# Performance work log

Measured on AMD Instinct MI355X. Metric: run time of the kernel, lower is better.

The kernel has to match this reference:

```python
import jax, jax.numpy as jnp
import numpy as np

NUM_HEADS = 8
D_MODEL = 512
D_K = D_MODEL // NUM_HEADS


def setup_inputs() -> dict:
    key = jax.random.key(0)
    ks = jax.random.split(key, 16)
    B, L, Dq = 4, 2048, 512
    s = 1.0 / np.sqrt(D_MODEL)
    inp = {
        "query": jax.random.normal(ks[0], (B, L, Dq), jnp.float32),
        "key": jax.random.normal(ks[1], (B, L, Dq), jnp.float32),
        "value": jax.random.normal(ks[2], (B, L, Dq), jnp.float32),
        "mask": jax.random.randint(ks[3], (B, L), 0, 2, jnp.int32),
        "Wq": jax.random.normal(ks[4], (Dq, D_MODEL), jnp.float32) * s,
        "bq": jax.random.normal(ks[5], (D_MODEL,), jnp.float32) * s,
        "Wk": jax.random.normal(ks[6], (Dq, D_MODEL), jnp.float32) * s,
        "bk": jax.random.normal(ks[7], (D_MODEL,), jnp.float32) * s,
        "Wv": jax.random.normal(ks[8], (Dq, D_MODEL), jnp.float32) * s,
        "bv": jax.random.normal(ks[9], (D_MODEL,), jnp.float32) * s,
        "Wo": jax.random.normal(ks[10], (D_MODEL, D_MODEL), jnp.float32) * s,
        "bo": jax.random.normal(ks[11], (D_MODEL,), jnp.float32) * s,
    }
    return inp


def _mha(query, key, value, mask, Wq, bq, Wk, bk, Wv, bv, Wo, bo):
    B, Q, _ = query.shape
    KV = key.shape[1]
    # projections, split into heads: (B, H, L, d_k)
    q = (query @ Wq + bq).reshape(B, Q, NUM_HEADS, D_K).transpose(0, 2, 1, 3)
    k = (key @ Wk + bk).reshape(B, KV, NUM_HEADS, D_K).transpose(0, 2, 1, 3)
    v = (value @ Wv + bv).reshape(B, KV, NUM_HEADS, D_K).transpose(0, 2, 1, 3)
    # full (B, H, Q, KV) score matrix, as in the original module
    scores = jnp.einsum("bhqd,bhkd->bhqk", q, k) / jnp.sqrt(jnp.asarray(D_K, q.dtype))
    m = (mask == 0)[:, None, None, :]  # (B,1,1,KV) broadcasting like unsqueeze(1)
    min_val = jnp.finfo(scores.dtype).min
    scores = jnp.where(m, min_val, scores)
    attn = jax.nn.softmax(scores, axis=-1)
    attn = jnp.where(m, 0.0, attn)
    xs = jnp.einsum("bhqk,bhkd->bhqd", attn, v)
    xs = xs.transpose(0, 2, 1, 3).reshape(B, Q, NUM_HEADS * D_K)
    return xs @ Wo + bo


def reference(query, key, value, mask, Wq, bq, Wk, bk, Wv, bv, Wo, bo):
    return _mha(query, key, value, mask, Wq, bq, Wk, bk, Wv, bv, Wo, bo)
```

## Files before the change

kernel.cpp:

```cpp
#include <hip/hip_runtime.h>
#include <math.h>

#define Bq 4
#define Lq 2048
#define NH 8
#define LDP6 36

typedef __attribute__((ext_vector_type(8))) __bf16 bf16x8;
typedef __attribute__((ext_vector_type(4))) float f32x4;
#define MFMA16(a,b,c) __builtin_amdgcn_mfma_f32_16x16x32_bf16(a,b,c,0,0,0)

__device__ __forceinline__ void async16(const void* g, void* l) {
    __builtin_amdgcn_global_load_lds(
        (const __attribute__((address_space(1))) unsigned int*)g,
        (__attribute__((address_space(3))) unsigned int*)l, 16, 0, 0);
}

__device__ __forceinline__ void splitbf(float x, ushort& h, ushort& l) {
    unsigned u = __float_as_uint(x);
    h = (ushort)(u >> 16);
    float hf = __uint_as_float(u & 0xffff0000u);
    l = (ushort)(__float_as_uint(x - hf) >> 16);
}
__device__ __forceinline__ ushort rnebf(float x) {
    unsigned u = __float_as_uint(x);
    return (ushort)((u + 0x7fffu + ((u >> 16) & 1u)) >> 16);
}

__global__ __launch_bounds__(256) void maskscan_kernel(
    const int* __restrict__ mask, int* __restrict__ idx, int* __restrict__ nvalid)
{
    __shared__ int ss[256];
    const int b = blockIdx.x, tid = threadIdx.x;
    int m[8], s = 0;
    #pragma unroll
    for (int j = 0; j < 8; ++j) { m[j] = (mask[b * 2048 + tid * 8 + j] != 0); s += m[j]; }
    int v = s;
    ss[tid] = v;
    __syncthreads();
    for (int off = 1; off < 256; off <<= 1) {
        int t_ = (tid >= off) ? ss[tid - off] : 0;
        __syncthreads();
        v += t_;
        ss[tid] = v;
        __syncthreads();
    }
    int pos = v - s;
    #pragma unroll
    for (int j = 0; j < 8; ++j) if (m[j]) idx[b * 2048 + pos++] = tid * 8 + j;
    int tot = ss[255];
    if (tid == 0) nvalid[b] = tot;
    for (int k = tot + tid; k < 2048; k += 256) idx[b * 2048 + k] = 0;
}

__global__ __launch_bounds__(256) void xsplit3_kernel(
    const float* __restrict__ X0, const float* __restrict__ X1, const float* __restrict__ X2,
    const int* __restrict__ idx,
    ushort* __restrict__ Xh, ushort* __restrict__ Xl)
{
    const int z = blockIdx.z;
    const float* X = (z == 0) ? X0 : (z == 1) ? X1 : X2;
    const size_t ebase = (size_t)blockIdx.x * 2048 + (size_t)threadIdx.x * 8;
    const int row = (int)(ebase >> 9), col = (int)(ebase & 511);
    const int b = row >> 11, r = row & 2047;
    const int srow = (z == 0) ? row : (b * 2048 + idx[b * 2048 + r]);
    const float* src = X + (size_t)srow * 512 + col;
    float4 a = *(const float4*)(src);
    float4 bb = *(const float4*)(src + 4);
    float vv[8] = {a.x, a.y, a.z, a.w, bb.x, bb.y, bb.z, bb.w};
    ushort hs[8], ls[8];
    #pragma unroll
    for (int j = 0; j < 8; ++j) splitbf(vv[j], hs[j], ls[j]);
    uint4 wh, wl;
    wh.x = hs[0] | ((unsigned)hs[1] << 16); wh.y = hs[2] | ((unsigned)hs[3] << 16);
    wh.z = hs[4] | ((unsigned)hs[5] << 16); wh.w = hs[6] | ((unsigned)hs[7] << 16);
    wl.x = ls[0] | ((unsigned)ls[1] << 16); wl.y = ls[2] | ((unsigned)ls[3] << 16);
    wl.z = ls[4] | ((unsigned)ls[5] << 16); wl.w = ls[6] | ((unsigned)ls[7] << 16);
    size_t off = (size_t)z * 8192 * 512 + ebase;
    *(uint4*)(Xh + off) = wh;
    *(uint4*)(Xl + off) = wl;
}

__global__ __launch_bounds__(256) void wsplit4_kernel(
    const float* __restrict__ W0, const float* __restrict__ W1,
    const float* __restrict__ W2, const float* __restrict__ W3,
    ushort* __restrict__ WTh, ushort* __restrict__ WTl)
{
    __shared__ float T[64][65];
    const int z = blockIdx.z;
    const float* W = (z == 0) ? W0 : (z == 1) ? W1 : (z == 2) ? W2 : W3;
    const int k0 = blockIdx.x * 64, n0 = blockIdx.y * 64;
    const int tid = threadIdx.x;
    #pragma unroll
    for (int i = 0; i < 4; ++i) {
        int u = tid + i * 256;
        int row = u >> 4, c4 = (u & 15) * 4;
        float4 v = *(const float4*)(W + (size_t)(k0 + row) * 512 + n0 + c4);
        T[row][c4 + 0] = v.x; T[row][c4 + 1] = v.y; T[row][c4 + 2] = v.z; T[row][c4 + 3] = v.w;
    }
    __syncthreads();
    #pragma unroll
    for (int i = 0; i < 2; ++i) {
        int u = tid + i * 256;
        int d = u >> 3, c8 = (u & 7) * 8;
        ushort hs[8], ls[8];
        #pragma unroll
        for (int j = 0; j < 8; ++j) splitbf(T[c8 + j][d], hs[j], ls[j]);
        uint4 wh, wl;
        wh.x = hs[0] | ((unsigned)hs[1] << 16); wh.y = hs[2] | ((unsigned)hs[3] << 16);
        wh.z = hs[4] | ((unsigned)hs[5] << 16); wh.w = hs[6] | ((unsigned)hs[7] << 16);
        wl.x = ls[0] | ((unsigned)ls[1] << 16); wl.y = ls[2] | ((unsigned)ls[3] << 16);
        wl.z = ls[4] | ((unsigned)ls[5] << 16); wl.w = ls[6] | ((unsigned)ls[7] << 16);
        size_t off = (size_t)(z * 512 + n0 + d) * 512 + k0 + c8;
        *(uint4*)(WTh + off) = wh;
        *(uint4*)(WTl + off) = wl;
    }
}

union GS {
    struct {
        ushort Ah[2][128 * 32];
        ushort Al[2][128 * 32];
        ushort Bh[2][2048];
        ushort Bl[2][2048];
    } s;
    ushort E[24576];
};

__global__ __launch_bounds__(256) void gemm2_kernel(
    const ushort* __restrict__ AhP, const ushort* __restrict__ AlP,
    const ushort* __restrict__ BhT, const ushort* __restrict__ BlT,
    const float* __restrict__ b0, const float* __restrict__ b1, const float* __restrict__ b2,
    const int* __restrict__ nvalid, int final_, float* __restrict__ Cf,
    ushort* __restrict__ Qh, ushort* __restrict__ Khp, ushort* __restrict__ VhT)
{
    __shared__ __align__(16) GS gs;
    const int tid = threadIdx.x;
    const int wave = tid >> 6, lane = tid & 63;
    const int l15 = lane & 15, quad = lane >> 4;
    const int m0 = blockIdx.x * 128;
    const int yy = blockIdx.y;
    const int mi = yy >> 3, n0 = (yy & 7) * 64;
    const int nglob = mi * 512 + n0;

    if (!final_ && mi >= 1) {
        int nv = nvalid[m0 >> 11];
        int nvpad = ((nv + 127) >> 7) << 7;
        if ((m0 & 2047) >= nvpad) return;
    }

    const float* bias = (mi == 0) ? b0 : (mi == 1) ? b1 : b2;
    const int wm = (wave & 1) * 64, wn = (wave >> 1) * 32;

    const ushort* AhZ = AhP + (size_t)mi * 8192 * 512;
    const ushort* AlZ = AlP + (size_t)mi * 8192 * 512;
    const int arow = lane >> 2;
    const int acsw = ((lane & 3) ^ ((lane >> 3) & 3)) * 8;
    const ushort* asrc[4]; int adst[4], apl[4];
    #pragma unroll
    for (int j = 0; j < 4; ++j) {
        int ri = wave * 4 + j, pl = ri >> 3, rb = ri & 7;
        asrc[j] = (pl ? AlZ : AhZ) + (size_t)(m0 + rb * 16 + arow) * 512 + acsw;
        adst[j] = rb * 512 + lane * 8;
        apl[j] = pl;
    }
    const int brow = lane >> 2, bsrc = (lane & 3) ^ (brow & 3);
    const ushort* bhp = BhT + (size_t)(nglob + wave * 16 + brow) * 512 + bsrc * 8;
    const ushort* blp = BlT + (size_t)(nglob + wave * 16 + brow) * 512 + bsrc * 8;
    const int bdst = wave * 512 + lane * 8;

    f32x4 acc[4][2];
    #pragma unroll
    for (int i = 0; i < 4; ++i)
        #pragma unroll
        for (int j = 0; j < 2; ++j) acc[i][j] = (f32x4){0.f, 0.f, 0.f, 0.f};

    #pragma unroll
    for (int j = 0; j < 4; ++j)
        async16(asrc[j], apl[j] ? &gs.s.Al[0][adst[j]] : &gs.s.Ah[0][adst[j]]);
    async16(bhp, &gs.s.Bh[0][bdst]);
    async16(blp, &gs.s.Bl[0][bdst]);

    for (int t = 0; t < 16; ++t) {
        const int p = t & 1;
        __syncthreads();
        if (t < 15) {
            const int kn = (t + 1) * 32;
            #pragma unroll
            for (int j = 0; j < 4; ++j)
                async16(asrc[j] + kn, apl[j] ? &gs.s.Al[1 - p][adst[j]] : &gs.s.Ah[1 - p][adst[j]]);
            async16(bhp + kn, &gs.s.Bh[1 - p][bdst]);
            async16(blp + kn, &gs.s.Bl[1 - p][bdst]);
        }
        bf16x8 afh[4], afl[4];
        #pragma unroll
        for (int ms = 0; ms < 4; ++ms) {
            int off = (wm + ms * 16 + l15) * 32 + (quad ^ ((l15 >> 1) & 3)) * 8;
            afh[ms] = *(const bf16x8*)&gs.s.Ah[p][off];
            afl[ms] = *(const bf16x8*)&gs.s.Al[p][off];
        }
        #pragma unroll
        for (int ns = 0; ns < 2; ++ns) {
            int off = (wn + ns * 16 + l15) * 32 + (quad ^ (l15 & 3)) * 8;
            bf16x8 bfh = *(const bf16x8*)&gs.s.Bh[p][off];
            bf16x8 bfl = *(const bf16x8*)&gs.s.Bl[p][off];
            #pragma unroll
            for (int ms = 0; ms < 4; ++ms) {
                acc[ms][ns] = MFMA16(afh[ms], bfl, acc[ms][ns]);
                acc[ms][ns] = MFMA16(afl[ms], bfh, acc[ms][ns]);
                acc[ms][ns] = MFMA16(afh[ms], bfh, acc[ms][ns]);
            }
        }
    }

    #pragma unroll
    for (int ns = 0; ns < 2; ++ns) {
        float bv = bias[n0 + wn + ns * 16 + l15];
        #pragma unroll
        for (int ms = 0; ms < 4; ++ms)
            #pragma unroll
            for (int r = 0; r < 4; ++r) acc[ms][ns][r] += bv;
    }

    if (final_) {
        #pragma unroll
        for (int ns = 0; ns < 2; ++ns) {
            int col = n0 + wn + ns * 16 + l15;
            #pragma unroll
            for (int ms = 0; ms < 4; ++ms)
                #pragma unroll
                for (int r = 0; r < 4; ++r)
                    Cf[(size_t)(m0 + wm + ms * 16 + quad * 4 + r) * 512 + col] = acc[ms][ns][r];
        }
        return;
    }

    const int h0 = n0 >> 6;
    const int b = m0 >> 11, rr0 = m0 & 2047;
    __syncthreads();
    #pragma unroll
    for (int ms = 0; ms < 4; ++ms) {
        #pragma unroll
        for (int ns = 0; ns < 2; ++ns) {
            int cl = wn + ns * 16 + l15;
            int rl = wm + ms * 16 + quad * 4;
            if (mi == 2) {
                ushort4 w4;
                #pragma unroll
                for (int r = 0; r < 4; ++r) ((ushort*)&w4)[r] = rnebf(acc[ms][ns][r]);
                *(ushort4*)&gs.E[cl * 136 + rl] = w4;
            } else {
                #pragma unroll
                for (int r = 0; r < 4; ++r) gs.E[(rl + r) * 72 + cl] = rnebf(acc[ms][ns][r]);
            }
        }
    }
    __syncthreads();
    if (mi == 2) {
        #pragma unroll
        for (int i = 0; i < 4; ++i) {
            int idx2 = tid + i * 256;
            int d = idx2 >> 4, rg = idx2 & 15;
            uint4 u = *(const uint4*)&gs.E[d * 136 + rg * 8];
            *(uint4*)&VhT[((size_t)(b * 8 + h0) * 64 + d) * 2048 + rr0 + rg * 8] = u;
        }
    } else {
        ushort* dst = (mi == 0) ? Qh : Khp;
        #pragma unroll
        for (int i = 0; i < 4; ++i) {
            int idx2 = tid + i * 256;
            int row = idx2 >> 3, cg = idx2 & 7;
            uint4 u = *(const uint4*)&gs.E[row * 72 + cg * 8];
            *(uint4*)&dst[((size_t)(b * 8 + h0) * 2048 + rr0 + row) * 64 + cg * 8] = u;
        }
    }
}

union SmemU {
    struct { ushort KVs[2][4][4096]; ushort Pp[8][64 * LDP6]; } p1;
    struct { float Obuf[4][64 * 68]; float Lbuf[4][64]; } p2;
};

__global__ __launch_bounds__(512, 2) void attn3_kernel(
    const ushort* __restrict__ Qh, const ushort* __restrict__ Kh,
    const ushort* __restrict__ VhT, const int* __restrict__ nvalid,
    ushort* __restrict__ XSh, ushort* __restrict__ XSl)
{
    __shared__ SmemU smem;
    const int tid = threadIdx.x;
    const int wave = tid >> 6, lane = tid & 63;
    const int l15 = lane & 15, quad = lane >> 4;
    const int w4 = wave & 3, half = wave >> 2;
    const int bh = blockIdx.x, b = bh >> 3, h = bh & 7;
    const int q0 = blockIdx.y * 256;

    const int nv = nvalid[b];
    const int nt = (nv + 127) >> 7;
    const int kvofs = half * 64 * nt;

    bf16x8 qf[4][2];
    #pragma unroll
    for (int qs = 0; qs < 4; ++qs) {
        size_t qb = ((size_t)bh * 2048 + q0 + w4 * 64 + qs * 16 + l15) * 64 + quad * 8;
        qf[qs][0] = *(const bf16x8*)(Qh + qb);
        qf[qs][1] = *(const bf16x8*)(Qh + qb + 32);
    }

    const f32x4 z = {0.f, 0.f, 0.f, 0.f};
    f32x4 oacc[4][4];
    #pragma unroll
    for (int i = 0; i < 4; ++i)
        #pragma unroll
        for (int j = 0; j < 4; ++j) oacc[i][j] = z;
    float lacc[4] = {0.f, 0.f, 0.f, 0.f};

    const int rloc = lane >> 3, gsw = (lane & 7) ^ rloc;
    const ushort* sb[4]; size_t sstep[4]; int dofs[4];
    #pragma unroll
    for (int i = 0; i < 4; ++i) {
        int cc = wave * 4 + i;
        int hc = cc >> 4, r16 = cc & 15, pc = r16 >> 3, ic = r16 & 7;
        if (pc == 0) {
            sb[i] = Kh + ((size_t)(bh * 2048 + hc * 64 * nt + ic * 8 + rloc)) * 64 + gsw * 8;
            sstep[i] = (size_t)64 * 64;
        } else {
            sb[i] = VhT + ((size_t)(bh * 64 + ic * 8 + rloc)) * 2048 + hc * 64 * nt + gsw * 8;
            sstep[i] = 64;
        }
        dofs[i] = (hc * 2 + pc) * 4096 + ic * 512;
    }

    const int sw0 = (quad ^ (l15 & 7)) * 8;
    const float SCL = 0.18033688011112042f;

    if (nt > 0) {
        #pragma unroll
        for (int i = 0; i < 4; ++i)
            async16(sb[i], &smem.p1.KVs[0][0][0] + dofs[i]);
    }

    for (int t = 0; t < nt; ++t) {
        __syncthreads();
        if (t + 1 < nt) {
            #pragma unroll
            for (int i = 0; i < 4; ++i)
                async16(sb[i] + (size_t)(t + 1) * sstep[i], &smem.p1.KVs[(t + 1) & 1][0][0] + dofs[i]);
        }
        const int p = t & 1;
        const ushort* K0 = smem.p1.KVs[p][half * 2 + 0];
        const ushort* V0 = smem.p1.KVs[p][half * 2 + 1];
        ushort* Pw = smem.p1.Pp[wave];

        #pragma unroll
        for (int ks = 0; ks < 2; ++ks) {
            #pragma unroll
            for (int kt2 = 0; kt2 < 2; ++kt2) {
                const int kt = ks * 2 + kt2;
                const int kb = (kt * 16 + l15) * 64;
                bf16x8 ka0 = *(const bf16x8*)&K0[kb + sw0];
                bf16x8 ka1 = *(const bf16x8*)&K0[kb + (sw0 ^ 32)];
                const int kbase = kvofs + t * 64 + kt * 16 + quad * 4;
                float bias[4];
                #pragma unroll
                for (int r = 0; r < 4; ++r) bias[r] = (kbase + r < nv) ? 0.f : -1e38f;
                #pragma unroll
                for (int qs = 0; qs < 4; ++qs) {
                    f32x4 a = z;
                    a = MFMA16(ka0, qf[qs][0], a);
                    a = MFMA16(ka1, qf[qs][1], a);
                    float pv[4];
                    #pragma unroll
                    for (int r = 0; r < 4; ++r) {
                        float x = __builtin_fmaf(a[r], SCL, bias[r]);
                        float e; asm("v_exp_f32 %0, %1" : "=v"(e) : "v"(x));
                        lacc[qs] += e;
                        pv[r] = e;
                    }
                    unsigned u01, u23;
                    asm("v_cvt_pk_bf16_f32 %0, %1, %2" : "=v"(u01) : "v"(pv[0]), "v"(pv[1]));
                    asm("v_cvt_pk_bf16_f32 %0, %1, %2" : "=v"(u23) : "v"(pv[2]), "v"(pv[3]));
                    uint2 w2; w2.x = u01; w2.y = u23;
                    *(uint2*)&Pw[(qs * 16 + l15) * LDP6 + kt2 * 16 + quad * 4] = w2;
                }
            }
            const int svo = sw0 ^ (ks * 32);
            bf16x8 pf[4];
            #pragma unroll
            for (int qs = 0; qs < 4; ++qs)
                pf[qs] = *(const bf16x8*)&Pw[(qs * 16 + l15) * LDP6 + quad * 8];
            #pragma unroll
            for (int dsub = 0; dsub < 4; ++dsub) {
                const int vb = (dsub * 16 + l15) * 64;
                bf16x8 vh = *(const bf16x8*)&V0[vb + svo];
                #pragma unroll
                for (int qs = 0; qs < 4; ++qs)
                    oacc[qs][dsub] = MFMA16(vh, pf[qs], oacc[qs][dsub]);
            }
        }
    }

    float lv[4];
    #pragma unroll
    for (int qs = 0; qs < 4; ++qs) {
        float v = lacc[qs];
        v += __shfl_xor(v, 16);
        v += __shfl_xor(v, 32);
        lv[qs] = v;
    }

    __syncthreads();
    if (half == 1) {
        #pragma unroll
        for (int qs = 0; qs < 4; ++qs) {
            #pragma unroll
            for (int dsub = 0; dsub < 4; ++dsub) {
                float4 o4 = {oacc[qs][dsub][0], oacc[qs][dsub][1], oacc[qs][dsub][2], oacc[qs][dsub][3]};
                *(float4*)&smem.p2.Obuf[w4][(qs * 16 + l15) * 68 + dsub * 16 + quad * 4] = o4;
            }
            if (quad == 0) smem.p2.Lbuf[w4][qs * 16 + l15] = lv[qs];
        }
    }
    __syncthreads();
    if (half == 0) {
        #pragma unroll
        for (int qs = 0; qs < 4; ++qs) {
            float ltot = lv[qs] + smem.p2.Lbuf[w4][qs * 16 + l15];
            float inv = (ltot > 0.f) ? 1.f / ltot : 0.f;
            int row = q0 + w4 * 64 + qs * 16 + l15;
            ushort* rph = XSh + ((size_t)(b * 2048 + row)) * 512 + h * 64;
            ushort* rpl = XSl + ((size_t)(b * 2048 + row)) * 512 + h * 64;
            #pragma unroll
            for (int dsub = 0; dsub < 4; ++dsub) {
                float4 p4 = *(const float4*)&smem.p2.Obuf[w4][(qs * 16 + l15) * 68 + dsub * 16 + quad * 4];
                float s0 = (oacc[qs][dsub][0] + p4.x) * inv;
                float s1 = (oacc[qs][dsub][1] + p4.y) * inv;
                float s2 = (oacc[qs][dsub][2] + p4.z) * inv;
                float s3 = (oacc[qs][dsub][3] + p4.w) * inv;
                ushort4 hv, lv4;
                splitbf(s0, hv.x, lv4.x); splitbf(s1, hv.y, lv4.y);
                splitbf(s2, hv.z, lv4.z); splitbf(s3, hv.w, lv4.w);
                *(ushort4*)&rph[dsub * 16 + quad * 4] = hv;
                *(ushort4*)&rpl[dsub * 16 + quad * 4] = lv4;
            }
        }
    }
}

extern "C" void kernel_launch(void* const* d_in, const int* in_sizes, int n_in,
                              void* d_out, int out_size, void* d_ws, size_t ws_size,
                              hipStream_t stream) {
    const float* query = (const float*)d_in[0];
    const float* key   = (const float*)d_in[1];
    const float* value = (const float*)d_in[2];
    const int*   mask  = (const int*)d_in[3];
    const float* Wq = (const float*)d_in[4];
    const float* bq = (const float*)d_in[5];
    const float* Wk = (const float*)d_in[6];
    const float* bk = (const float*)d_in[7];
    const float* Wv = (const float*)d_in[8];
    const float* bv = (const float*)d_in[9];
    const float* Wo = (const float*)d_in[10];
    const float* bo = (const float*)d_in[11];

    char* w = (char*)d_ws;
    const size_t MB = (size_t)1 << 20;
    ushort* Qh  = (ushort*)(w + 0 * MB);
    ushort* Khp = (ushort*)(w + 16 * MB);
    ushort* VhT = (ushort*)(w + 24 * MB);
    ushort* Xh3 = (ushort*)(w + 40 * MB);
    ushort* Xl3 = (ushort*)(w + 64 * MB);
    ushort* XSh = (ushort*)(w + 56 * MB);
    ushort* XSl = (ushort*)(w + 64 * MB);
    ushort* WTh = (ushort*)(w + 88 * MB);
    ushort* WTl = (ushort*)(w + 90 * MB);
    int* idxbuf = (int*)(w + 92 * MB);
    int* nvbuf  = (int*)(w + 92 * MB + 65536);

    maskscan_kernel<<<dim3(4), 256, 0, stream>>>(mask, idxbuf, nvbuf);
    xsplit3_kernel<<<dim3(2048, 1, 3), 256, 0, stream>>>(query, key, value, idxbuf, Xh3, Xl3);
    wsplit4_kernel<<<dim3(8, 8, 4), 256, 0, stream>>>(Wq, Wk, Wv, Wo, WTh, WTl);
    gemm2_kernel<<<dim3(64, 24), 256, 0, stream>>>(
        Xh3, Xl3, WTh, WTl, bq, bk, bv, nvbuf, 0, nullptr, Qh, Khp, VhT);
    attn3_kernel<<<dim3(32, 8), 512, 0, stream>>>(Qh, Khp, VhT, nvbuf, XSh, XSl);
    gemm2_kernel<<<dim3(64, 8), 256, 0, stream>>>(
        XSh, XSl, WTh + (size_t)1536 * 512, WTl + (size_t)1536 * 512,
        bo, bo, bo, nvbuf, 1, (float*)d_out,
        nullptr, nullptr, nullptr);
}
```

Baseline: 222.5 us.

## Drop activation low-part split, widen GEMM tile to 128 columns, skip padded rows

Activations (inputs and the attention output) are now rounded to a single bf16 plane instead of being split into high and low bf16 parts, so each GEMM step issues two MFMAs instead of three and the A-operand traffic is halved. The GEMM tile grows from 128x64 to 128x128, with each wave covering 64 columns, to improve reuse of the A tile, and the epilogue writes two heads per block. The conversion kernel also skips gathered key and value rows beyond the padded valid count. This lowers accuracy because activations lose their low-order correction term, and it raises register pressure in the GEMM.

```diff
diff --git a/kernel.cpp b/kernel.cpp
--- a/kernel.cpp
+++ b/kernel.cpp
@@ -53,32 +53,33 @@
     for (int k = tot + tid; k < 2048; k += 256) idx[b * 2048 + k] = 0;
 }
 
-__global__ __launch_bounds__(256) void xsplit3_kernel(
+__global__ __launch_bounds__(256) void xrne3_kernel(
     const float* __restrict__ X0, const float* __restrict__ X1, const float* __restrict__ X2,
-    const int* __restrict__ idx,
-    ushort* __restrict__ Xh, ushort* __restrict__ Xl)
+    const int* __restrict__ idx, const int* __restrict__ nvalid,
+    ushort* __restrict__ Xr)
 {
     const int z = blockIdx.z;
     const float* X = (z == 0) ? X0 : (z == 1) ? X1 : X2;
     const size_t ebase = (size_t)blockIdx.x * 2048 + (size_t)threadIdx.x * 8;
     const int row = (int)(ebase >> 9), col = (int)(ebase & 511);
     const int b = row >> 11, r = row & 2047;
+    if (z >= 1) {
+        int nv = nvalid[b];
+        int nvpad = ((nv + 127) >> 7) << 7;
+        if (r >= nvpad) return;
+    }
     const int srow = (z == 0) ? row : (b * 2048 + idx[b * 2048 + r]);
     const float* src = X + (size_t)srow * 512 + col;
     float4 a = *(const float4*)(src);
     float4 bb = *(const float4*)(src + 4);
     float vv[8] = {a.x, a.y, a.z, a.w, bb.x, bb.y, bb.z, bb.w};
-    ushort hs[8], ls[8];
-    #pragma unroll
-    for (int j = 0; j < 8; ++j) splitbf(vv[j], hs[j], ls[j]);
-    uint4 wh, wl;
+    ushort hs[8];
+    #pragma unroll
+    for (int j = 0; j < 8; ++j) hs[j] = rnebf(vv[j]);
+    uint4 wh;
     wh.x = hs[0] | ((unsigned)hs[1] << 16); wh.y = hs[2] | ((unsigned)hs[3] << 16);
     wh.z = hs[4] | ((unsigned)hs[5] << 16); wh.w = hs[6] | ((unsigned)hs[7] << 16);
-    wl.x = ls[0] | ((unsigned)ls[1] << 16); wl.y = ls[2] | ((unsigned)ls[3] << 16);
-    wl.z = ls[4] | ((unsigned)ls[5] << 16); wl.w = ls[6] | ((unsigned)ls[7] << 16);
-    size_t off = (size_t)z * 8192 * 512 + ebase;
-    *(uint4*)(Xh + off) = wh;
-    *(uint4*)(Xl + off) = wl;
+    *(uint4*)(Xr + (size_t)z * 8192 * 512 + ebase) = wh;
 }
 
 __global__ __launch_bounds__(256) void wsplit4_kernel(
@@ -119,16 +120,15 @@
 
 union GS {
     struct {
-        ushort Ah[2][128 * 32];
-        ushort Al[2][128 * 32];
-        ushort Bh[2][2048];
-        ushort Bl[2][2048];
+        ushort A[2][4096];
+        ushort Bh[2][4096];
+        ushort Bl[2][4096];
     } s;
     ushort E[24576];
 };
 
 __global__ __launch_bounds__(256) void gemm2_kernel(
-    const ushort* __restrict__ AhP, const ushort* __restrict__ AlP,
+    const ushort* __restrict__ Ap,
     const ushort* __restrict__ BhT, const ushort* __restrict__ BlT,
     const float* __restrict__ b0, const float* __restrict__ b1, const float* __restrict__ b2,
     const int* __restrict__ nvalid, int final_, float* __restrict__ Cf,
@@ -140,7 +140,7 @@
     const int l15 = lane & 15, quad = lane >> 4;
     const int m0 = blockIdx.x * 128;
     const int yy = blockIdx.y;
-    const int mi = yy >> 3, n0 = (yy & 7) * 64;
+    const int mi = yy >> 2, n0 = (yy & 3) * 128;
     const int nglob = mi * 512 + n0;
 
     if (!final_ && mi >= 1) {
@@ -150,36 +150,41 @@
     }
 
     const float* bias = (mi == 0) ? b0 : (mi == 1) ? b1 : b2;
-    const int wm = (wave & 1) * 64, wn = (wave >> 1) * 32;
-
-    const ushort* AhZ = AhP + (size_t)mi * 8192 * 512;
-    const ushort* AlZ = AlP + (size_t)mi * 8192 * 512;
+    const int wm = (wave & 1) * 64, wn = (wave >> 1) * 64;
+
+    const ushort* AZ = Ap + (size_t)mi * 8192 * 512;
     const int arow = lane >> 2;
-    const int acsw = ((lane & 3) ^ ((lane >> 3) & 3)) * 8;
-    const ushort* asrc[4]; int adst[4], apl[4];
-    #pragma unroll
-    for (int j = 0; j < 4; ++j) {
-        int ri = wave * 4 + j, pl = ri >> 3, rb = ri & 7;
-        asrc[j] = (pl ? AlZ : AhZ) + (size_t)(m0 + rb * 16 + arow) * 512 + acsw;
+    const int acs = ((lane & 3) ^ ((arow >> 1) & 3)) * 8;
+    const ushort* asrc[2]; int adst[2];
+    #pragma unroll
+    for (int j = 0; j < 2; ++j) {
+        int rb = wave * 2 + j;
+        asrc[j] = AZ + (size_t)(m0 + rb * 16 + arow) * 512 + acs;
         adst[j] = rb * 512 + lane * 8;
-        apl[j] = pl;
-    }
-    const int brow = lane >> 2, bsrc = (lane & 3) ^ (brow & 3);
-    const ushort* bhp = BhT + (size_t)(nglob + wave * 16 + brow) * 512 + bsrc * 8;
-    const ushort* blp = BlT + (size_t)(nglob + wave * 16 + brow) * 512 + bsrc * 8;
-    const int bdst = wave * 512 + lane * 8;
-
-    f32x4 acc[4][2];
+    }
+    const int brow = lane >> 2;
+    const int bcs = ((lane & 3) ^ (brow & 3)) * 8;
+    const ushort* bsh[2]; const ushort* bsl[2]; int bdst[2];
+    #pragma unroll
+    for (int j = 0; j < 2; ++j) {
+        int r2 = wave * 32 + j * 16 + brow;
+        bsh[j] = BhT + (size_t)(nglob + r2) * 512 + bcs;
+        bsl[j] = BlT + (size_t)(nglob + r2) * 512 + bcs;
+        bdst[j] = wave * 1024 + j * 512 + lane * 8;
+    }
+
+    f32x4 acc[4][4];
     #pragma unroll
     for (int i = 0; i < 4; ++i)
         #pragma unroll
-        for (int j = 0; j < 2; ++j) acc[i][j] = (f32x4){0.f, 0.f, 0.f, 0.f};
-
-    #pragma unroll
-    for (int j = 0; j < 4; ++j)
-        async16(asrc[j], apl[j] ? &gs.s.Al[0][adst[j]] : &gs.s.Ah[0][adst[j]]);
-    async16(bhp, &gs.s.Bh[0][bdst]);
-    async16(blp, &gs.s.Bl[0][bdst]);
+        for (int j = 0; j < 4; ++j) acc[i][j] = (f32x4){0.f, 0.f, 0.f, 0.f};
+
+    #pragma unroll
+    for (int j = 0; j < 2; ++j) {
+        async16(asrc[j], &gs.s.A[0][adst[j]]);
+        async16(bsh[j], &gs.s.Bh[0][bdst[j]]);
+        async16(bsl[j], &gs.s.Bl[0][bdst[j]]);
+    }
 
     for (int t = 0; t < 16; ++t) {
         const int p = t & 1;
@@ -187,34 +192,33 @@
         if (t < 15) {
             const int kn = (t + 1) * 32;
             #pragma unroll
-            for (int j = 0; j < 4; ++j)
-                async16(asrc[j] + kn, apl[j] ? &gs.s.Al[1 - p][adst[j]] : &gs.s.Ah[1 - p][adst[j]]);
-            async16(bhp + kn, &gs.s.Bh[1 - p][bdst]);
-            async16(blp + kn, &gs.s.Bl[1 - p][bdst]);
-        }
-        bf16x8 afh[4], afl[4];
+            for (int j = 0; j < 2; ++j) {
+                async16(asrc[j] + kn, &gs.s.A[1 - p][adst[j]]);
+                async16(bsh[j] + kn, &gs.s.Bh[1 - p][bdst[j]]);
+                async16(bsl[j] + kn, &gs.s.Bl[1 - p][bdst[j]]);
+            }
+        }
+        bf16x8 af[4];
         #pragma unroll
         for (int ms = 0; ms < 4; ++ms) {
             int off = (wm + ms * 16 + l15) * 32 + (quad ^ ((l15 >> 1) & 3)) * 8;
-            afh[ms] = *(const bf16x8*)&gs.s.Ah[p][off];
-            afl[ms] = *(const bf16x8*)&gs.s.Al[p][off];
-        }
-        #pragma unroll
-        for (int ns = 0; ns < 2; ++ns) {
+            af[ms] = *(const bf16x8*)&gs.s.A[p][off];
+        }
+        #pragma unroll
+        for (int ns = 0; ns < 4; ++ns) {
             int off = (wn + ns * 16 + l15) * 32 + (quad ^ (l15 & 3)) * 8;
             bf16x8 bfh = *(const bf16x8*)&gs.s.Bh[p][off];
             bf16x8 bfl = *(const bf16x8*)&gs.s.Bl[p][off];
             #pragma unroll
             for (int ms = 0; ms < 4; ++ms) {
-                acc[ms][ns] = MFMA16(afh[ms], bfl, acc[ms][ns]);
-                acc[ms][ns] = MFMA16(afl[ms], bfh, acc[ms][ns]);
-                acc[ms][ns] = MFMA16(afh[ms], bfh, acc[ms][ns]);
-            }
-        }
-    }
-
-    #pragma unroll
-    for (int ns = 0; ns < 2; ++ns) {
+                acc[ms][ns] = MFMA16(af[ms], bfl, acc[ms][ns]);
+                acc[ms][ns] = MFMA16(af[ms], bfh, acc[ms][ns]);
+            }
+        }
+    }
+
+    #pragma unroll
+    for (int ns = 0; ns < 4; ++ns) {
         float bv = bias[n0 + wn + ns * 16 + l15];
         #pragma unroll
         for (int ms = 0; ms < 4; ++ms)
@@ -224,7 +228,7 @@
 
     if (final_) {
         #pragma unroll
-        for (int ns = 0; ns < 2; ++ns) {
+        for (int ns = 0; ns < 4; ++ns) {
             int col = n0 + wn + ns * 16 + l15;
             #pragma unroll
             for (int ms = 0; ms < 4; ++ms)
@@ -241,7 +245,7 @@
     #pragma unroll
     for (int ms = 0; ms < 4; ++ms) {
         #pragma unroll
-        for (int ns = 0; ns < 2; ++ns) {
+        for (int ns = 0; ns < 4; ++ns) {
             int cl = wn + ns * 16 + l15;
             int rl = wm + ms * 16 + quad * 4;
             if (mi == 2) {
@@ -251,27 +255,29 @@
                 *(ushort4*)&gs.E[cl * 136 + rl] = w4;
             } else {
                 #pragma unroll
-                for (int r = 0; r < 4; ++r) gs.E[(rl + r) * 72 + cl] = rnebf(acc[ms][ns][r]);
+                for (int r = 0; r < 4; ++r) gs.E[(rl + r) * 136 + cl] = rnebf(acc[ms][ns][r]);
             }
         }
     }
     __syncthreads();
     if (mi == 2) {
         #pragma unroll
-        for (int i = 0; i < 4; ++i) {
+        for (int i = 0; i < 8; ++i) {
             int idx2 = tid + i * 256;
             int d = idx2 >> 4, rg = idx2 & 15;
+            int head = d >> 6, dd = d & 63;
             uint4 u = *(const uint4*)&gs.E[d * 136 + rg * 8];
-            *(uint4*)&VhT[((size_t)(b * 8 + h0) * 64 + d) * 2048 + rr0 + rg * 8] = u;
+            *(uint4*)&VhT[((size_t)(b * 8 + h0 + head) * 64 + dd) * 2048 + rr0 + rg * 8] = u;
         }
     } else {
         ushort* dst = (mi == 0) ? Qh : Khp;
         #pragma unroll
-        for (int i = 0; i < 4; ++i) {
+        for (int i = 0; i < 8; ++i) {
             int idx2 = tid + i * 256;
-            int row = idx2 >> 3, cg = idx2 & 7;
-            uint4 u = *(const uint4*)&gs.E[row * 72 + cg * 8];
-            *(uint4*)&dst[((size_t)(b * 8 + h0) * 2048 + rr0 + row) * 64 + cg * 8] = u;
+            int row = idx2 >> 4, cg = idx2 & 15;
+            int head = cg >> 3, c8 = (cg & 7) * 8;
+            uint4 u = *(const uint4*)&gs.E[row * 136 + cg * 8];
+            *(uint4*)&dst[((size_t)(b * 8 + h0 + head) * 2048 + rr0 + row) * 64 + c8] = u;
         }
     }
 }
@@ -284,7 +290,7 @@
 __global__ __launch_bounds__(512, 2) void attn3_kernel(
     const ushort* __restrict__ Qh, const ushort* __restrict__ Kh,
     const ushort* __restrict__ VhT, const int* __restrict__ nvalid,
-    ushort* __restrict__ XSh, ushort* __restrict__ XSl)
+    ushort* __restrict__ XS)
 {
     __shared__ SmemU smem;
     const int tid = threadIdx.x;
@@ -427,20 +433,16 @@
             float ltot = lv[qs] + smem.p2.Lbuf[w4][qs * 16 + l15];
             float inv = (ltot > 0.f) ? 1.f / ltot : 0.f;
             int row = q0 + w4 * 64 + qs * 16 + l15;
-            ushort* rph = XSh + ((size_t)(b * 2048 + row)) * 512 + h * 64;
-            ushort* rpl = XSl + ((size_t)(b * 2048 + row)) * 512 + h * 64;
+            ushort* rp = XS + ((size_t)(b * 2048 + row)) * 512 + h * 64;
             #pragma unroll
             for (int dsub = 0; dsub < 4; ++dsub) {
                 float4 p4 = *(const float4*)&smem.p2.Obuf[w4][(qs * 16 + l15) * 68 + dsub * 16 + quad * 4];
-                float s0 = (oacc[qs][dsub][0] + p4.x) * inv;
-                float s1 = (oacc[qs][dsub][1] + p4.y) * inv;
-                float s2 = (oacc[qs][dsub][2] + p4.z) * inv;
-                float s3 = (oacc[qs][dsub][3] + p4.w) * inv;
-                ushort4 hv, lv4;
-                splitbf(s0, hv.x, lv4.x); splitbf(s1, hv.y, lv4.y);
-                splitbf(s2, hv.z, lv4.z); splitbf(s3, hv.w, lv4.w);
-                *(ushort4*)&rph[dsub * 16 + quad * 4] = hv;
-                *(ushort4*)&rpl[dsub * 16 + quad * 4] = lv4;
+                ushort4 hv;
+                hv.x = rnebf((oacc[qs][dsub][0] + p4.x) * inv);
+                hv.y = rnebf((oacc[qs][dsub][1] + p4.y) * inv);
+                hv.z = rnebf((oacc[qs][dsub][2] + p4.z) * inv);
+                hv.w = rnebf((oacc[qs][dsub][3] + p4.w) * inv);
+                *(ushort4*)&rp[dsub * 16 + quad * 4] = hv;
             }
         }
     }
@@ -465,25 +467,23 @@
     char* w = (char*)d_ws;
     const size_t MB = (size_t)1 << 20;
     ushort* Qh  = (ushort*)(w + 0 * MB);
+    ushort* XS  = (ushort*)(w + 8 * MB);
     ushort* Khp = (ushort*)(w + 16 * MB);
     ushort* VhT = (ushort*)(w + 24 * MB);
-    ushort* Xh3 = (ushort*)(w + 40 * MB);
-    ushort* Xl3 = (ushort*)(w + 64 * MB);
-    ushort* XSh = (ushort*)(w + 56 * MB);
-    ushort* XSl = (ushort*)(w + 64 * MB);
-    ushort* WTh = (ushort*)(w + 88 * MB);
-    ushort* WTl = (ushort*)(w + 90 * MB);
-    int* idxbuf = (int*)(w + 92 * MB);
-    int* nvbuf  = (int*)(w + 92 * MB + 65536);
+    ushort* Xr  = (ushort*)(w + 32 * MB);
+    ushort* WTh = (ushort*)(w + 80 * MB);
+    ushort* WTl = (ushort*)(w + 82 * MB);
+    int* idxbuf = (int*)(w + 84 * MB);
+    int* nvbuf  = (int*)(w + 84 * MB + 65536);
 
     maskscan_kernel<<<dim3(4), 256, 0, stream>>>(mask, idxbuf, nvbuf);
-    xsplit3_kernel<<<dim3(2048, 1, 3), 256, 0, stream>>>(query, key, value, idxbuf, Xh3, Xl3);
+    xrne3_kernel<<<dim3(2048, 1, 3), 256, 0, stream>>>(query, key, value, idxbuf, nvbuf, Xr);
     wsplit4_kernel<<<dim3(8, 8, 4), 256, 0, stream>>>(Wq, Wk, Wv, Wo, WTh, WTl);
-    gemm2_kernel<<<dim3(64, 24), 256, 0, stream>>>(
-        Xh3, Xl3, WTh, WTl, bq, bk, bv, nvbuf, 0, nullptr, Qh, Khp, VhT);
-    attn3_kernel<<<dim3(32, 8), 512, 0, stream>>>(Qh, Khp, VhT, nvbuf, XSh, XSl);
-    gemm2_kernel<<<dim3(64, 8), 256, 0, stream>>>(
-        XSh, XSl, WTh + (size_t)1536 * 512, WTl + (size_t)1536 * 512,
+    gemm2_kernel<<<dim3(64, 12), 256, 0, stream>>>(
+        Xr, WTh, WTl, bq, bk, bv, nvbuf, 0, nullptr, Qh, Khp, VhT);
+    attn3_kernel<<<dim3(32, 8), 512, 0, stream>>>(Qh, Khp, VhT, nvbuf, XS);
+    gemm2_kernel<<<dim3(64, 4), 256, 0, stream>>>(
+        XS, WTh + (size_t)1536 * 512, WTl + (size_t)1536 * 512,
         bo, bo, bo, nvbuf, 1, (float*)d_out,
         nullptr, nullptr, nullptr);
 }
```

New measurement: 203.7 us. 8.4% less time.
